# Kernel tuning notes

Hardware: AMD Instinct MI355X
Metric: run time of the kernel (lower is better)

Reference implementation:

```python
import jax, jax.numpy as jnp
import numpy as np

VOCAB, EMBED, HIDDEN = 256, 512, 1024
B, T = 64, 512


def setup_inputs() -> dict:
    key = jax.random.key(0)
    ks = jax.random.split(key, 12)
    s = 0.02
    return {
        "x": jax.random.randint(ks[0], (B, T), 0, VOCAB),
        "embed": jax.random.normal(ks[1], (VOCAB, EMBED), jnp.float32) * s,
        "Wih0": jax.random.normal(ks[2], (3 * HIDDEN, EMBED), jnp.float32) * s,
        "Whh0": jax.random.normal(ks[3], (3 * HIDDEN, HIDDEN), jnp.float32) * s,
        "bih0": jax.random.normal(ks[4], (3 * HIDDEN,), jnp.float32) * s,
        "bhh0": jax.random.normal(ks[5], (3 * HIDDEN,), jnp.float32) * s,
        "Wih1": jax.random.normal(ks[6], (3 * HIDDEN, HIDDEN), jnp.float32) * s,
        "Whh1": jax.random.normal(ks[7], (3 * HIDDEN, HIDDEN), jnp.float32) * s,
        "bih1": jax.random.normal(ks[8], (3 * HIDDEN,), jnp.float32) * s,
        "bhh1": jax.random.normal(ks[9], (3 * HIDDEN,), jnp.float32) * s,
        "W_out": jax.random.normal(ks[10], (VOCAB, HIDDEN), jnp.float32) * s,
        "b_out": jax.random.normal(ks[11], (VOCAB,), jnp.float32) * s,
    }


def gru_cell(inp, h, Wih, Whh, bih, bhh):
    # PyTorch GRUCell math.
    gi = inp @ Wih.T + bih  # (B, 3H)
    gh = h @ Whh.T + bhh    # (B, 3H)
    i_r, i_z, i_n = jnp.split(gi, 3, axis=-1)
    h_r, h_z, h_n = jnp.split(gh, 3, axis=-1)
    r = jax.nn.sigmoid(i_r + h_r)
    z = jax.nn.sigmoid(i_z + h_z)
    n = jnp.tanh(i_n + r * h_n)
    return (1.0 - z) * n + z * h


def reference(x, embed, Wih0, Whh0, bih0, bhh0, Wih1, Whh1, bih1, bhh1, W_out, b_out):
    emb = embed[x]                       # (B, T, E)
    xs = jnp.swapaxes(emb, 0, 1)         # (T, B, E)
    h0 = jnp.zeros((x.shape[0], HIDDEN), emb.dtype)

    def step(carry, inp_t):
        h_0, h_1 = carry
        h_0 = gru_cell(inp_t, h_0, Wih0, Whh0, bih0, bhh0)
        h_1 = gru_cell(h_0, h_1, Wih1, Whh1, bih1, bhh1)
        return (h_0, h_1), h_1

    _, outs = jax.lax.scan(step, (h0, h0), xs)   # outs: (T, B, H)
    outs = jnp.swapaxes(outs, 0, 1)              # (B, T, H)
    logits = outs @ W_out.T + b_out              # (B, T, V)
    return logits
```

## Files before the change

### kernel.cpp

```cpp
#include <hip/hip_runtime.h>
#include <stdint.h>

typedef short short8 __attribute__((ext_vector_type(8)));
typedef float f32x4 __attribute__((ext_vector_type(4)));
typedef unsigned short u16;

#define MFMA16(a, b, c) __builtin_amdgcn_mfma_f32_16x16x32_bf16((a), (b), (c), 0, 0, 0)

#define T_LEN 512
#define BATCH 64
#define EMB_D 512
#define HID 1024
#define VOC 256
#define NWG 128
#define RNN_THREADS 512
#define R0 256
#define R1 8
#define SLOT (BATCH * HID)

#define OFF_XT    0u
#define OFF_EMBT  131072u
#define OFF_WIH0  524288u
#define OFF_WHH0  3670016u
#define OFF_WIH1  9961472u
#define OFF_WHH1  16252928u
#define OFF_WOUT  22544384u
#define OFF_H0R   23068672u
#define OFF_H1R   56623104u
#define OFF_H1ALL 57671680u
#define OFF_SYNC  124780544u
#define SYNC_BYTES 16640u
#define WS_TOTAL  (OFF_SYNC + SYNC_BYTES)

static __device__ __forceinline__ u16 f2b(float f) {
  uint32_t u = __float_as_uint(f);
  u += 0x7FFFu + ((u >> 16) & 1u);
  return (u16)(u >> 16);
}
static __device__ __forceinline__ float sigm(float x) { return 1.0f / (1.0f + __expf(-x)); }

__global__ void cvt_kernel(const float* __restrict__ src, u16* __restrict__ dst, int n) {
  int i = ((int)blockIdx.x * 256 + (int)threadIdx.x) * 4;
  if (i + 4 <= n) {
    const float4 v = *(const float4*)(src + i);
    ushort4 o;
    o.x = f2b(v.x); o.y = f2b(v.y); o.z = f2b(v.z); o.w = f2b(v.w);
    *(ushort4*)(dst + i) = o;
  }
}

__global__ void xt_kernel(const int* __restrict__ x, int* __restrict__ xT) {
  const int t = (int)blockIdx.x, b = (int)threadIdx.x;
  xT[t * BATCH + b] = x[b * T_LEN + t];
}

static __device__ __forceinline__ void poll_flags(unsigned* p0, unsigned* p1,
                                                  unsigned t0, unsigned t1, int tid) {
  if (tid < 128) {
    unsigned* f = (tid < 64) ? (p0 + (size_t)tid * 32) : (p1 + (size_t)(tid - 64) * 32);
    const unsigned tgt = (tid < 64) ? t0 : t1;
    while (__hip_atomic_load(f, __ATOMIC_RELAXED, __HIP_MEMORY_SCOPE_AGENT) < tgt)
      __builtin_amdgcn_s_sleep(1);
  }
  __syncthreads();
}

__global__ __launch_bounds__(RNN_THREADS, 1) void rnn_persist_kernel(
    const int* __restrict__ xT, const u16* __restrict__ embtab,
    const u16* __restrict__ A0i_r, const u16* __restrict__ A0i_z, const u16* __restrict__ A0i_n,
    const u16* __restrict__ A0h_r, const u16* __restrict__ A0h_z, const u16* __restrict__ A0h_n,
    const u16* __restrict__ A1i_r, const u16* __restrict__ A1i_z, const u16* __restrict__ A1i_n,
    const u16* __restrict__ A1h_r, const u16* __restrict__ A1h_z, const u16* __restrict__ A1h_n,
    const float* __restrict__ bih0, const float* __restrict__ bhh0,
    const float* __restrict__ bih1, const float* __restrict__ bhh1,
    u16* __restrict__ h0r, u16* __restrict__ h1r,
    u16* __restrict__ h1all, unsigned* __restrict__ sync)
{
  __shared__ __align__(16) float lds[16384];
  const int tid = (int)threadIdx.x;
  const int wv = tid >> 6;
  const int lane = tid & 63;
  const int lrow = lane & 15;
  const int lk8 = (lane >> 4) << 3;
  const int wgid = (int)blockIdx.x;
  const int layer = wgid >> 6;
  const int ubase = (wgid & 63) << 4;
  const bool iwave = (wv < 4);
  const bool l0i = (layer == 0) && iwave;
  unsigned* p0 = sync;
  unsigned* p1 = sync + 64 * 32;

  const u16 *Ar, *Az, *An;
  int ldb, k0;
  if (layer == 0) {
    if (iwave) { Ar = A0i_r; Az = A0i_z; An = A0i_n; ldb = EMB_D; k0 = wv * 128; }
    else       { Ar = A0h_r; Az = A0h_z; An = A0h_n; ldb = HID;   k0 = (wv - 4) * 256; }
  } else {
    if (iwave) { Ar = A1i_r; Az = A1i_z; An = A1i_n; ldb = HID;   k0 = wv * 256; }
    else       { Ar = A1h_r; Az = A1h_z; An = A1h_n; ldb = HID;   k0 = (wv - 4) * 256; }
  }
  const size_t arow = (size_t)(ubase + lrow) * ldb;

  const float* bi = layer ? bih1 : bih0;
  const float* bh = layer ? bhh1 : bhh0;
  const int u0 = (tid & 7) * 2;
  const int eb = tid >> 3;
  const int eug0 = ubase + u0, eug1 = eug0 + 1;
  const float bR0 = bi[eug0] + bh[eug0];
  const float bZ0 = bi[HID + eug0] + bh[HID + eug0];
  const float bNi0 = bi[2 * HID + eug0];
  const float bNh0 = bh[2 * HID + eug0];
  const float bR1 = bi[eug1] + bh[eug1];
  const float bZ1 = bi[HID + eug1] + bh[HID + eug1];
  const float bNi1 = bi[2 * HID + eug1];
  const float bNh1 = bh[2 * HID + eug1];
  const int l_e = ((u0 >> 2) << 4) | (eb & 15);
  const int r0 = u0 & 3, r1 = r0 + 1;
  const int ebt = eb >> 4;
  const int ix0 = l_e ^ (r0 << 3), ix1 = l_e ^ (r1 << 3);
  float hp0 = 0.f, hp1 = 0.f;

  const int sBeg = (layer == 0) ? 0 : 1;
  const int sEnd = (layer == 0) ? (T_LEN - 1) : T_LEN;

  for (int s = sBeg; s <= sEnd; ++s) {
    if (layer == 0) {
      const unsigned bp = (s >= 252) ? (unsigned)(s - 250) : 0u;
      poll_flags(p0, p1, (unsigned)s, bp, tid);
    } else {
      poll_flags(p0, p1, (unsigned)s, (unsigned)(s - 1), tid);
    }

    unsigned packed;
    {
      const u16* h0prev = h0r + (size_t)((s - 1) & (R0 - 1)) * SLOT;
      const u16* h1prev = h1r + (size_t)((s - 2) & (R1 - 1)) * SLOT;

      f32x4 acc0[4], acc1[4], accn[4];
#pragma unroll
      for (int bt = 0; bt < 4; ++bt) {
        acc0[bt] = (f32x4){0.f, 0.f, 0.f, 0.f};
        acc1[bt] = (f32x4){0.f, 0.f, 0.f, 0.f};
        accn[bt] = (f32x4){0.f, 0.f, 0.f, 0.f};
      }
      if (l0i) {
        const u16* brow[4];
#pragma unroll
        for (int bt = 0; bt < 4; ++bt) {
          const int tok = xT[s * BATCH + bt * 16 + lrow];
          brow[bt] = embtab + (size_t)tok * EMB_D;
        }
        short8 bfr[4][4];
#pragma unroll
        for (int ks = 0; ks < 4; ++ks)
#pragma unroll
          for (int bt = 0; bt < 4; ++bt)
            bfr[bt][ks] = *(const short8*)(brow[bt] + k0 + ks * 32 + lk8);
#pragma unroll
        for (int ks = 0; ks < 4; ++ks) {
          const int kk = k0 + ks * 32 + lk8;
          const short8 ar = *(const short8*)(Ar + arow + kk);
          const short8 az = *(const short8*)(Az + arow + kk);
          const short8 an = *(const short8*)(An + arow + kk);
#pragma unroll
          for (int bt = 0; bt < 4; ++bt) {
            acc0[bt] = MFMA16(ar, bfr[bt][ks], acc0[bt]);
            acc1[bt] = MFMA16(az, bfr[bt][ks], acc1[bt]);
            accn[bt] = MFMA16(an, bfr[bt][ks], accn[bt]);
          }
        }
      } else {
        const u16* Bp;
        if (layer == 0) Bp = h0prev;
        else            Bp = iwave ? h0prev : h1prev;
        short8 bfr[4][8];
#pragma unroll
        for (int ks = 0; ks < 8; ++ks)
#pragma unroll
          for (int bt = 0; bt < 4; ++bt)
            bfr[bt][ks] = *(const short8*)(Bp + (size_t)(bt * 16 + lrow) * HID + k0 + ks * 32 + lk8);
#pragma unroll
        for (int ks = 0; ks < 8; ++ks) {
          const int kk = k0 + ks * 32 + lk8;
          const short8 ar = *(const short8*)(Ar + arow + kk);
          const short8 az = *(const short8*)(Az + arow + kk);
          const short8 an = *(const short8*)(An + arow + kk);
#pragma unroll
          for (int bt = 0; bt < 4; ++bt) {
            acc0[bt] = MFMA16(ar, bfr[bt][ks], acc0[bt]);
            acc1[bt] = MFMA16(az, bfr[bt][ks], acc1[bt]);
            accn[bt] = MFMA16(an, bfr[bt][ks], accn[bt]);
          }
        }
      }
      if (iwave) {
#pragma unroll
        for (int bt = 0; bt < 4; ++bt)
#pragma unroll
          for (int r = 0; r < 4; ++r) {
            const int ix = lane ^ (r << 3);
            lds[(((wv * 4 + 0) * 4 + bt) * 256) + r * 64 + ix] = acc0[bt][r];
            lds[(((wv * 4 + 1) * 4 + bt) * 256) + r * 64 + ix] = acc1[bt][r];
            lds[(((wv * 4 + 2) * 4 + bt) * 256) + r * 64 + ix] = accn[bt][r];
          }
      }
      __syncthreads();
      if (!iwave) {
        const int z = wv - 4;
#pragma unroll
        for (int bt = 0; bt < 4; ++bt)
#pragma unroll
          for (int r = 0; r < 4; ++r) {
            const int ix = lane ^ (r << 3);
            float* q0 = &lds[(((z * 4 + 0) * 4 + bt) * 256) + r * 64 + ix];
            float* q1 = &lds[(((z * 4 + 1) * 4 + bt) * 256) + r * 64 + ix];
            *q0 = *q0 + acc0[bt][r];
            *q1 = *q1 + acc1[bt][r];
            lds[(((z * 4 + 3) * 4 + bt) * 256) + r * 64 + ix] = accn[bt][r];
          }
      }
      __syncthreads();
      {
        float sr0 = 0.f, sz0 = 0.f, sni0 = 0.f, snh0 = 0.f;
        float sr1 = 0.f, sz1 = 0.f, sni1 = 0.f, snh1 = 0.f;
#pragma unroll
        for (int z = 0; z < 4; ++z) {
          sr0  += lds[(((z * 4 + 0) * 4 + ebt) * 256) + r0 * 64 + ix0];
          sz0  += lds[(((z * 4 + 1) * 4 + ebt) * 256) + r0 * 64 + ix0];
          sni0 += lds[(((z * 4 + 2) * 4 + ebt) * 256) + r0 * 64 + ix0];
          snh0 += lds[(((z * 4 + 3) * 4 + ebt) * 256) + r0 * 64 + ix0];
          sr1  += lds[(((z * 4 + 0) * 4 + ebt) * 256) + r1 * 64 + ix1];
          sz1  += lds[(((z * 4 + 1) * 4 + ebt) * 256) + r1 * 64 + ix1];
          sni1 += lds[(((z * 4 + 2) * 4 + ebt) * 256) + r1 * 64 + ix1];
          snh1 += lds[(((z * 4 + 3) * 4 + ebt) * 256) + r1 * 64 + ix1];
        }
        const float rg0 = sigm(sr0 + bR0);
        const float zg0 = sigm(sz0 + bZ0);
        const float ng0 = tanhf(sni0 + bNi0 + rg0 * (snh0 + bNh0));
        const float hn0 = (1.0f - zg0) * ng0 + zg0 * hp0;
        const float rg1 = sigm(sr1 + bR1);
        const float zg1 = sigm(sz1 + bZ1);
        const float ng1 = tanhf(sni1 + bNi1 + rg1 * (snh1 + bNh1));
        const float hn1 = (1.0f - zg1) * ng1 + zg1 * hp1;
        hp0 = hn0; hp1 = hn1;
        packed = (unsigned)f2b(hn0) | ((unsigned)f2b(hn1) << 16);
        u16* wslot = layer ? (h1r + (size_t)((s - 1) & (R1 - 1)) * SLOT)
                           : (h0r + (size_t)(s & (R0 - 1)) * SLOT);
        __hip_atomic_store((unsigned*)&wslot[eb * HID + eug0], packed,
                           __ATOMIC_RELAXED, __HIP_MEMORY_SCOPE_AGENT);
      }
    }
    __syncthreads();
    if (tid == 0) {
      unsigned* f = layer ? (p1 + (size_t)(wgid - 64) * 32) : (p0 + (size_t)wgid * 32);
      __hip_atomic_store(f, (unsigned)(s + (layer ? 0 : 1)), __ATOMIC_RELAXED,
                         __HIP_MEMORY_SCOPE_AGENT);
    }
    if (layer)
      *(unsigned*)&h1all[((size_t)(s - 1) * BATCH + eb) * HID + eug0] = packed;
  }
}

__global__ __launch_bounds__(256, 2) void logits_kernel(
    const u16* __restrict__ h1all, const u16* __restrict__ Woutb,
    const float* __restrict__ bout, float* __restrict__ out)
{
  __shared__ __align__(16) short lds[16 * 4 * 64 * 8];
  const int tid = (int)threadIdx.x;
  const int wv = tid >> 6, lane = tid & 63;
  const int lrow = lane & 15, lk8 = (lane >> 4) << 3;
  const int row0 = (int)blockIdx.x * 64 + wv * 16;
  f32x4 acc[16];
#pragma unroll
  for (int i = 0; i < 16; ++i) acc[i] = (f32x4){0.f, 0.f, 0.f, 0.f};

  for (int kc = 0; kc < HID; kc += 128) {
    __syncthreads();
#pragma unroll
    for (int j = 0; j < 16; ++j) {
      const int slot = tid + j * 256;
      const int ct = slot >> 8, kt = (slot >> 6) & 3, l = slot & 63;
      *(short8*)&lds[slot * 8] =
          *(const short8*)(Woutb + (size_t)(ct * 16 + (l & 15)) * HID + kc + kt * 32 + ((l >> 4) << 3));
    }
    __syncthreads();
#pragma unroll
    for (int kt = 0; kt < 4; ++kt) {
      const short8 af = *(const short8*)(h1all + (size_t)(row0 + lrow) * HID + kc + kt * 32 + lk8);
#pragma unroll
      for (int ct = 0; ct < 16; ++ct) {
        const short8 bf = *(const short8*)&lds[((ct * 4 + kt) * 64 + lane) * 8];
        acc[ct] = MFMA16(af, bf, acc[ct]);
      }
    }
  }
#pragma unroll
  for (int ct = 0; ct < 16; ++ct) {
    const int v = ct * 16 + lrow;
    const float bo = bout[v];
#pragma unroll
    for (int r = 0; r < 4; ++r) {
      const int row = row0 + (lane >> 4) * 4 + r;
      const int t = row >> 6, b = row & 63;
      out[((size_t)(b * T_LEN + t)) * VOC + v] = acc[ct][r] + bo;
    }
  }
}

extern "C" void kernel_launch(void* const* d_in, const int* in_sizes, int n_in,
                              void* d_out, int out_size, void* d_ws, size_t ws_size,
                              hipStream_t stream) {
  const int*   x     = (const int*)d_in[0];
  const float* embed = (const float*)d_in[1];
  const float* Wih0  = (const float*)d_in[2];
  const float* Whh0  = (const float*)d_in[3];
  const float* bih0  = (const float*)d_in[4];
  const float* bhh0  = (const float*)d_in[5];
  const float* Wih1  = (const float*)d_in[6];
  const float* Whh1  = (const float*)d_in[7];
  const float* bih1  = (const float*)d_in[8];
  const float* bhh1  = (const float*)d_in[9];
  const float* Wout  = (const float*)d_in[10];
  const float* bout  = (const float*)d_in[11];
  float* out = (float*)d_out;
  char* ws = (char*)d_ws;
  if (ws_size < (size_t)WS_TOTAL) return;

  hipMemsetAsync(ws + OFF_H0R + (size_t)(R0 - 1) * SLOT * 2, 0, SLOT * 2, stream);
  hipMemsetAsync(ws + OFF_H1R + (size_t)(R1 - 1) * SLOT * 2, 0, SLOT * 2, stream);
  hipMemsetAsync(ws + OFF_SYNC, 0, SYNC_BYTES, stream);
  xt_kernel<<<512, 64, 0, stream>>>(x, (int*)(ws + OFF_XT));
  cvt_kernel<<<128, 256, 0, stream>>>(embed, (u16*)(ws + OFF_EMBT), 256 * 512);
  cvt_kernel<<<1536, 256, 0, stream>>>(Wih0, (u16*)(ws + OFF_WIH0), 3072 * 512);
  cvt_kernel<<<3072, 256, 0, stream>>>(Whh0, (u16*)(ws + OFF_WHH0), 3072 * 1024);
  cvt_kernel<<<3072, 256, 0, stream>>>(Wih1, (u16*)(ws + OFF_WIH1), 3072 * 1024);
  cvt_kernel<<<3072, 256, 0, stream>>>(Whh1, (u16*)(ws + OFF_WHH1), 3072 * 1024);
  cvt_kernel<<<256, 256, 0, stream>>>(Wout, (u16*)(ws + OFF_WOUT), 256 * 1024);

  const u16* wih0b = (const u16*)(ws + OFF_WIH0);
  const u16* whh0b = (const u16*)(ws + OFF_WHH0);
  const u16* wih1b = (const u16*)(ws + OFF_WIH1);
  const u16* whh1b = (const u16*)(ws + OFF_WHH1);

  rnn_persist_kernel<<<NWG, RNN_THREADS, 0, stream>>>(
      (const int*)(ws + OFF_XT), (const u16*)(ws + OFF_EMBT),
      wih0b, wih0b + 524288, wih0b + 1048576,
      whh0b, whh0b + 1048576, whh0b + 2097152,
      wih1b, wih1b + 1048576, wih1b + 2097152,
      whh1b, whh1b + 1048576, whh1b + 2097152,
      bih0, bhh0, bih1, bhh1,
      (u16*)(ws + OFF_H0R), (u16*)(ws + OFF_H1R),
      (u16*)(ws + OFF_H1ALL), (unsigned*)(ws + OFF_SYNC));

  logits_kernel<<<512, 256, 0, stream>>>((const u16*)(ws + OFF_H1ALL),
                                         (const u16*)(ws + OFF_WOUT), bout, out);
}
```

Baseline: 7.805 ms.

## Split GRU matvecs across all waves and overlap independent work with flag polling

Each wave now computes both input and hidden contributions over a smaller K slice instead of dedicating waves to input vs hidden paths, and the work that does not depend on the awaited hidden state (the embedding projection for layer 0, the recurrent h1 term for layer 1) is issued before the corresponding flag wait. Layer 1 waits on its two dependencies separately so it can start on h1prev before layer 0 finishes. The new hidden state is staged through LDS and written with 128 coalesced dwordx4 stores carrying sc0 sc1 cache bits instead of scattered per-thread atomic stores. This aims to shorten the per-step critical path of the persistent recurrent kernel, at the cost of extra barriers and a four-way LDS reduction.

```diff
diff --git a/kernel.cpp b/kernel.cpp
--- a/kernel.cpp
+++ b/kernel.cpp
@@ -3,6 +3,7 @@
 
 typedef short short8 __attribute__((ext_vector_type(8)));
 typedef float f32x4 __attribute__((ext_vector_type(4)));
+typedef int int4v __attribute__((ext_vector_type(4)));
 typedef unsigned short u16;
 
 #define MFMA16(a, b, c) __builtin_amdgcn_mfma_f32_16x16x32_bf16((a), (b), (c), 0, 0, 0)
@@ -52,17 +53,6 @@
 __global__ void xt_kernel(const int* __restrict__ x, int* __restrict__ xT) {
   const int t = (int)blockIdx.x, b = (int)threadIdx.x;
   xT[t * BATCH + b] = x[b * T_LEN + t];
-}
-
-static __device__ __forceinline__ void poll_flags(unsigned* p0, unsigned* p1,
-                                                  unsigned t0, unsigned t1, int tid) {
-  if (tid < 128) {
-    unsigned* f = (tid < 64) ? (p0 + (size_t)tid * 32) : (p1 + (size_t)(tid - 64) * 32);
-    const unsigned tgt = (tid < 64) ? t0 : t1;
-    while (__hip_atomic_load(f, __ATOMIC_RELAXED, __HIP_MEMORY_SCOPE_AGENT) < tgt)
-      __builtin_amdgcn_s_sleep(1);
-  }
-  __syncthreads();
 }
 
 __global__ __launch_bounds__(RNN_THREADS, 1) void rnn_persist_kernel(
@@ -85,21 +75,19 @@
   const int wgid = (int)blockIdx.x;
   const int layer = wgid >> 6;
   const int ubase = (wgid & 63) << 4;
-  const bool iwave = (wv < 4);
-  const bool l0i = (layer == 0) && iwave;
   unsigned* p0 = sync;
   unsigned* p1 = sync + 64 * 32;
 
-  const u16 *Ar, *Az, *An;
-  int ldb, k0;
-  if (layer == 0) {
-    if (iwave) { Ar = A0i_r; Az = A0i_z; An = A0i_n; ldb = EMB_D; k0 = wv * 128; }
-    else       { Ar = A0h_r; Az = A0h_z; An = A0h_n; ldb = HID;   k0 = (wv - 4) * 256; }
-  } else {
-    if (iwave) { Ar = A1i_r; Az = A1i_z; An = A1i_n; ldb = HID;   k0 = wv * 256; }
-    else       { Ar = A1h_r; Az = A1h_z; An = A1h_n; ldb = HID;   k0 = (wv - 4) * 256; }
-  }
-  const size_t arow = (size_t)(ubase + lrow) * ldb;
+  const u16 *Axr, *Axz, *Axn, *Ahr, *Ahz, *Ahn;
+  int ldx;
+  if (layer == 0) { Axr = A0i_r; Axz = A0i_z; Axn = A0i_n;
+                    Ahr = A0h_r; Ahz = A0h_z; Ahn = A0h_n; ldx = EMB_D; }
+  else            { Axr = A1i_r; Axz = A1i_z; Axn = A1i_n;
+                    Ahr = A1h_r; Ahz = A1h_z; Ahn = A1h_n; ldx = HID; }
+  const size_t axrow = (size_t)(ubase + lrow) * ldx;
+  const size_t ahrow = (size_t)(ubase + lrow) * HID;
+  const int k0e = wv * 64;
+  const int k0h = wv * 128;
 
   const float* bi = layer ? bih1 : bih0;
   const float* bh = layer ? bhh1 : bhh0;
@@ -124,131 +112,180 @@
   const int sEnd = (layer == 0) ? (T_LEN - 1) : T_LEN;
 
   for (int s = sBeg; s <= sEnd; ++s) {
+    const u16* h0prev = h0r + (size_t)((s - 1) & (R0 - 1)) * SLOT;
+    const u16* h1prev = h1r + (size_t)((s - 2) & (R1 - 1)) * SLOT;
+
+    f32x4 aR[4], aZ[4], aNi[4], aNh[4];
+#pragma unroll
+    for (int bt = 0; bt < 4; ++bt) {
+      aR[bt] = (f32x4){0.f, 0.f, 0.f, 0.f};
+      aZ[bt] = (f32x4){0.f, 0.f, 0.f, 0.f};
+      aNi[bt] = (f32x4){0.f, 0.f, 0.f, 0.f};
+      aNh[bt] = (f32x4){0.f, 0.f, 0.f, 0.f};
+    }
+
     if (layer == 0) {
-      const unsigned bp = (s >= 252) ? (unsigned)(s - 250) : 0u;
-      poll_flags(p0, p1, (unsigned)s, bp, tid);
+      const u16* brow[4];
+#pragma unroll
+      for (int bt = 0; bt < 4; ++bt) {
+        const int tok = xT[s * BATCH + bt * 16 + lrow];
+        brow[bt] = embtab + (size_t)tok * EMB_D;
+      }
+#pragma unroll
+      for (int ks = 0; ks < 2; ++ks) {
+        const int kk = k0e + ks * 32 + lk8;
+        const short8 ar = *(const short8*)(Axr + axrow + kk);
+        const short8 az = *(const short8*)(Axz + axrow + kk);
+        const short8 an = *(const short8*)(Axn + axrow + kk);
+#pragma unroll
+        for (int bt = 0; bt < 4; ++bt) {
+          const short8 bf = *(const short8*)(brow[bt] + kk);
+          aR[bt] = MFMA16(ar, bf, aR[bt]);
+          aZ[bt] = MFMA16(az, bf, aZ[bt]);
+          aNi[bt] = MFMA16(an, bf, aNi[bt]);
+        }
+      }
+      if (tid < 128) {
+        unsigned* f; unsigned tgt;
+        if (tid < 64) { f = p0 + (size_t)tid * 32; tgt = (unsigned)s; }
+        else { f = p1 + (size_t)(tid - 64) * 32;
+               tgt = (s >= 252) ? (unsigned)(s - 250) : 0u; }
+        while (__hip_atomic_load(f, __ATOMIC_RELAXED, __HIP_MEMORY_SCOPE_AGENT) < tgt)
+          __builtin_amdgcn_s_sleep(1);
+      }
+      __syncthreads();
+#pragma unroll
+      for (int ks = 0; ks < 4; ++ks) {
+        const int kk = k0h + ks * 32 + lk8;
+        const short8 ar = *(const short8*)(Ahr + ahrow + kk);
+        const short8 az = *(const short8*)(Ahz + ahrow + kk);
+        const short8 an = *(const short8*)(Ahn + ahrow + kk);
+#pragma unroll
+        for (int bt = 0; bt < 4; ++bt) {
+          const short8 bf = *(const short8*)(h0prev + (size_t)(bt * 16 + lrow) * HID + kk);
+          aR[bt] = MFMA16(ar, bf, aR[bt]);
+          aZ[bt] = MFMA16(az, bf, aZ[bt]);
+          aNh[bt] = MFMA16(an, bf, aNh[bt]);
+        }
+      }
     } else {
-      poll_flags(p0, p1, (unsigned)s, (unsigned)(s - 1), tid);
-    }
+      if (tid >= 64 && tid < 128) {
+        unsigned* f = p1 + (size_t)(tid - 64) * 32;
+        const unsigned tgt = (unsigned)(s - 1);
+        while (__hip_atomic_load(f, __ATOMIC_RELAXED, __HIP_MEMORY_SCOPE_AGENT) < tgt)
+          __builtin_amdgcn_s_sleep(1);
+      }
+      __syncthreads();
+#pragma unroll
+      for (int ks = 0; ks < 4; ++ks) {
+        const int kk = k0h + ks * 32 + lk8;
+        const short8 ar = *(const short8*)(Ahr + ahrow + kk);
+        const short8 az = *(const short8*)(Ahz + ahrow + kk);
+        const short8 an = *(const short8*)(Ahn + ahrow + kk);
+#pragma unroll
+        for (int bt = 0; bt < 4; ++bt) {
+          const short8 bf = *(const short8*)(h1prev + (size_t)(bt * 16 + lrow) * HID + kk);
+          aR[bt] = MFMA16(ar, bf, aR[bt]);
+          aZ[bt] = MFMA16(az, bf, aZ[bt]);
+          aNh[bt] = MFMA16(an, bf, aNh[bt]);
+        }
+      }
+      if (tid < 64) {
+        unsigned* f = p0 + (size_t)tid * 32;
+        const unsigned tgt = (unsigned)s;
+        while (__hip_atomic_load(f, __ATOMIC_RELAXED, __HIP_MEMORY_SCOPE_AGENT) < tgt)
+          __builtin_amdgcn_s_sleep(1);
+      }
+      __syncthreads();
+#pragma unroll
+      for (int ks = 0; ks < 4; ++ks) {
+        const int kk = k0h + ks * 32 + lk8;
+        const short8 ar = *(const short8*)(Axr + axrow + kk);
+        const short8 az = *(const short8*)(Axz + axrow + kk);
+        const short8 an = *(const short8*)(Axn + axrow + kk);
+#pragma unroll
+        for (int bt = 0; bt < 4; ++bt) {
+          const short8 bf = *(const short8*)(h0prev + (size_t)(bt * 16 + lrow) * HID + kk);
+          aR[bt] = MFMA16(ar, bf, aR[bt]);
+          aZ[bt] = MFMA16(az, bf, aZ[bt]);
+          aNi[bt] = MFMA16(an, bf, aNi[bt]);
+        }
+      }
+    }
+
+    if (wv < 4) {
+#pragma unroll
+      for (int bt = 0; bt < 4; ++bt)
+#pragma unroll
+        for (int r = 0; r < 4; ++r) {
+          const int ix = lane ^ (r << 3);
+          lds[(((wv * 4 + 0) * 4 + bt) * 256) + r * 64 + ix] = aR[bt][r];
+          lds[(((wv * 4 + 1) * 4 + bt) * 256) + r * 64 + ix] = aZ[bt][r];
+          lds[(((wv * 4 + 2) * 4 + bt) * 256) + r * 64 + ix] = aNi[bt][r];
+          lds[(((wv * 4 + 3) * 4 + bt) * 256) + r * 64 + ix] = aNh[bt][r];
+        }
+    }
+    __syncthreads();
+    if (wv >= 4) {
+      const int z = wv - 4;
+#pragma unroll
+      for (int bt = 0; bt < 4; ++bt)
+#pragma unroll
+        for (int r = 0; r < 4; ++r) {
+          const int ix = lane ^ (r << 3);
+          float* q0 = &lds[(((z * 4 + 0) * 4 + bt) * 256) + r * 64 + ix];
+          float* q1 = &lds[(((z * 4 + 1) * 4 + bt) * 256) + r * 64 + ix];
+          float* q2 = &lds[(((z * 4 + 2) * 4 + bt) * 256) + r * 64 + ix];
+          float* q3 = &lds[(((z * 4 + 3) * 4 + bt) * 256) + r * 64 + ix];
+          *q0 = *q0 + aR[bt][r];
+          *q1 = *q1 + aZ[bt][r];
+          *q2 = *q2 + aNi[bt][r];
+          *q3 = *q3 + aNh[bt][r];
+        }
+    }
+    __syncthreads();
 
     unsigned packed;
     {
-      const u16* h0prev = h0r + (size_t)((s - 1) & (R0 - 1)) * SLOT;
-      const u16* h1prev = h1r + (size_t)((s - 2) & (R1 - 1)) * SLOT;
-
-      f32x4 acc0[4], acc1[4], accn[4];
-#pragma unroll
-      for (int bt = 0; bt < 4; ++bt) {
-        acc0[bt] = (f32x4){0.f, 0.f, 0.f, 0.f};
-        acc1[bt] = (f32x4){0.f, 0.f, 0.f, 0.f};
-        accn[bt] = (f32x4){0.f, 0.f, 0.f, 0.f};
-      }
-      if (l0i) {
-        const u16* brow[4];
-#pragma unroll
-        for (int bt = 0; bt < 4; ++bt) {
-          const int tok = xT[s * BATCH + bt * 16 + lrow];
-          brow[bt] = embtab + (size_t)tok * EMB_D;
-        }
-        short8 bfr[4][4];
-#pragma unroll
-        for (int ks = 0; ks < 4; ++ks)
-#pragma unroll
-          for (int bt = 0; bt < 4; ++bt)
-            bfr[bt][ks] = *(const short8*)(brow[bt] + k0 + ks * 32 + lk8);
-#pragma unroll
-        for (int ks = 0; ks < 4; ++ks) {
-          const int kk = k0 + ks * 32 + lk8;
-          const short8 ar = *(const short8*)(Ar + arow + kk);
-          const short8 az = *(const short8*)(Az + arow + kk);
-          const short8 an = *(const short8*)(An + arow + kk);
-#pragma unroll
-          for (int bt = 0; bt < 4; ++bt) {
-            acc0[bt] = MFMA16(ar, bfr[bt][ks], acc0[bt]);
-            acc1[bt] = MFMA16(az, bfr[bt][ks], acc1[bt]);
-            accn[bt] = MFMA16(an, bfr[bt][ks], accn[bt]);
-          }
-        }
-      } else {
-        const u16* Bp;
-        if (layer == 0) Bp = h0prev;
-        else            Bp = iwave ? h0prev : h1prev;
-        short8 bfr[4][8];
-#pragma unroll
-        for (int ks = 0; ks < 8; ++ks)
-#pragma unroll
-          for (int bt = 0; bt < 4; ++bt)
-            bfr[bt][ks] = *(const short8*)(Bp + (size_t)(bt * 16 + lrow) * HID + k0 + ks * 32 + lk8);
-#pragma unroll
-        for (int ks = 0; ks < 8; ++ks) {
-          const int kk = k0 + ks * 32 + lk8;
-          const short8 ar = *(const short8*)(Ar + arow + kk);
-          const short8 az = *(const short8*)(Az + arow + kk);
-          const short8 an = *(const short8*)(An + arow + kk);
-#pragma unroll
-          for (int bt = 0; bt < 4; ++bt) {
-            acc0[bt] = MFMA16(ar, bfr[bt][ks], acc0[bt]);
-            acc1[bt] = MFMA16(az, bfr[bt][ks], acc1[bt]);
-            accn[bt] = MFMA16(an, bfr[bt][ks], accn[bt]);
-          }
-        }
-      }
-      if (iwave) {
-#pragma unroll
-        for (int bt = 0; bt < 4; ++bt)
-#pragma unroll
-          for (int r = 0; r < 4; ++r) {
-            const int ix = lane ^ (r << 3);
-            lds[(((wv * 4 + 0) * 4 + bt) * 256) + r * 64 + ix] = acc0[bt][r];
-            lds[(((wv * 4 + 1) * 4 + bt) * 256) + r * 64 + ix] = acc1[bt][r];
-            lds[(((wv * 4 + 2) * 4 + bt) * 256) + r * 64 + ix] = accn[bt][r];
-          }
-      }
-      __syncthreads();
-      if (!iwave) {
-        const int z = wv - 4;
-#pragma unroll
-        for (int bt = 0; bt < 4; ++bt)
-#pragma unroll
-          for (int r = 0; r < 4; ++r) {
-            const int ix = lane ^ (r << 3);
-            float* q0 = &lds[(((z * 4 + 0) * 4 + bt) * 256) + r * 64 + ix];
-            float* q1 = &lds[(((z * 4 + 1) * 4 + bt) * 256) + r * 64 + ix];
-            *q0 = *q0 + acc0[bt][r];
-            *q1 = *q1 + acc1[bt][r];
-            lds[(((z * 4 + 3) * 4 + bt) * 256) + r * 64 + ix] = accn[bt][r];
-          }
-      }
-      __syncthreads();
-      {
-        float sr0 = 0.f, sz0 = 0.f, sni0 = 0.f, snh0 = 0.f;
-        float sr1 = 0.f, sz1 = 0.f, sni1 = 0.f, snh1 = 0.f;
-#pragma unroll
-        for (int z = 0; z < 4; ++z) {
-          sr0  += lds[(((z * 4 + 0) * 4 + ebt) * 256) + r0 * 64 + ix0];
-          sz0  += lds[(((z * 4 + 1) * 4 + ebt) * 256) + r0 * 64 + ix0];
-          sni0 += lds[(((z * 4 + 2) * 4 + ebt) * 256) + r0 * 64 + ix0];
-          snh0 += lds[(((z * 4 + 3) * 4 + ebt) * 256) + r0 * 64 + ix0];
-          sr1  += lds[(((z * 4 + 0) * 4 + ebt) * 256) + r1 * 64 + ix1];
-          sz1  += lds[(((z * 4 + 1) * 4 + ebt) * 256) + r1 * 64 + ix1];
-          sni1 += lds[(((z * 4 + 2) * 4 + ebt) * 256) + r1 * 64 + ix1];
-          snh1 += lds[(((z * 4 + 3) * 4 + ebt) * 256) + r1 * 64 + ix1];
-        }
-        const float rg0 = sigm(sr0 + bR0);
-        const float zg0 = sigm(sz0 + bZ0);
-        const float ng0 = tanhf(sni0 + bNi0 + rg0 * (snh0 + bNh0));
-        const float hn0 = (1.0f - zg0) * ng0 + zg0 * hp0;
-        const float rg1 = sigm(sr1 + bR1);
-        const float zg1 = sigm(sz1 + bZ1);
-        const float ng1 = tanhf(sni1 + bNi1 + rg1 * (snh1 + bNh1));
-        const float hn1 = (1.0f - zg1) * ng1 + zg1 * hp1;
-        hp0 = hn0; hp1 = hn1;
-        packed = (unsigned)f2b(hn0) | ((unsigned)f2b(hn1) << 16);
-        u16* wslot = layer ? (h1r + (size_t)((s - 1) & (R1 - 1)) * SLOT)
-                           : (h0r + (size_t)(s & (R0 - 1)) * SLOT);
-        __hip_atomic_store((unsigned*)&wslot[eb * HID + eug0], packed,
-                           __ATOMIC_RELAXED, __HIP_MEMORY_SCOPE_AGENT);
-      }
+      float sr0 = 0.f, sz0 = 0.f, sni0 = 0.f, snh0 = 0.f;
+      float sr1 = 0.f, sz1 = 0.f, sni1 = 0.f, snh1 = 0.f;
+#pragma unroll
+      for (int z = 0; z < 4; ++z) {
+        sr0  += lds[(((z * 4 + 0) * 4 + ebt) * 256) + r0 * 64 + ix0];
+        sz0  += lds[(((z * 4 + 1) * 4 + ebt) * 256) + r0 * 64 + ix0];
+        sni0 += lds[(((z * 4 + 2) * 4 + ebt) * 256) + r0 * 64 + ix0];
+        snh0 += lds[(((z * 4 + 3) * 4 + ebt) * 256) + r0 * 64 + ix0];
+        sr1  += lds[(((z * 4 + 0) * 4 + ebt) * 256) + r1 * 64 + ix1];
+        sz1  += lds[(((z * 4 + 1) * 4 + ebt) * 256) + r1 * 64 + ix1];
+        sni1 += lds[(((z * 4 + 2) * 4 + ebt) * 256) + r1 * 64 + ix1];
+        snh1 += lds[(((z * 4 + 3) * 4 + ebt) * 256) + r1 * 64 + ix1];
+      }
+      const float rg0 = sigm(sr0 + bR0);
+      const float zg0 = sigm(sz0 + bZ0);
+      const float ng0 = tanhf(sni0 + bNi0 + rg0 * (snh0 + bNh0));
+      const float hn0 = (1.0f - zg0) * ng0 + zg0 * hp0;
+      const float rg1 = sigm(sr1 + bR1);
+      const float zg1 = sigm(sz1 + bZ1);
+      const float ng1 = tanhf(sni1 + bNi1 + rg1 * (snh1 + bNh1));
+      const float hn1 = (1.0f - zg1) * ng1 + zg1 * hp1;
+      hp0 = hn0; hp1 = hn1;
+      packed = (unsigned)f2b(hn0) | ((unsigned)f2b(hn1) << 16);
+    }
+    __syncthreads();
+    {
+      u16* stag = (u16*)lds;
+      *(unsigned*)&stag[eb * 16 + u0] = packed;
+    }
+    __syncthreads();
+    u16* wslot = layer ? (h1r + (size_t)((s - 1) & (R1 - 1)) * SLOT)
+                       : (h0r + (size_t)(s & (R0 - 1)) * SLOT);
+    if (tid < 128) {
+      const int b = tid >> 1, half = tid & 1;
+      const int4v d = *(const int4v*)((const char*)lds + b * 32 + half * 16);
+      const unsigned long long dst =
+          (unsigned long long)(uintptr_t)(wslot + (size_t)b * HID + ubase + half * 8);
+      asm volatile("global_store_dwordx4 %0, %1, off sc0 sc1"
+                   :: "v"(dst), "v"(d) : "memory");
     }
     __syncthreads();
     if (tid == 0) {
```

New measurement: 8.025 ms. 1.03x slower.
